# Kernel optimization log

Measured on AMD Instinct MI355X. Metric: run time of the kernel, lower is better.

The kernel has to match this reference:

```python
import jax, jax.numpy as jnp
import numpy as np

EPS = 1e-6

def rmsnorm(x, w):
    # x: (B, N, D), w: (D,)
    var = jnp.mean(jnp.square(x), axis=-1, keepdims=True)
    return x * jax.lax.rsqrt(var + EPS) * w

def head_mixing(x):
    # Parameter-free cross-head mix: split each head's D dims into N chunks
    # and transpose the (head, chunk) axes. x: (B, N, D), D % N == 0.
    B, N, D = x.shape
    c = D // N
    return x.reshape(B, N, N, c).transpose(0, 2, 1, 3).reshape(B, N, D)

def setup_inputs() -> dict:
    key = jax.random.key(0)
    ks = jax.random.split(key, 4)
    B, N, D, H = 8192, 16, 256, 512
    return {
        "x": jax.random.normal(ks[0], (B, N, D), dtype=jnp.float32),
        "norm1_w": jnp.ones((D,), dtype=jnp.float32),
        "norm2_w": jnp.ones((D,), dtype=jnp.float32),
        "w1": jax.random.normal(ks[1], (N, D, H), dtype=jnp.float32) * (1.0 / np.sqrt(D)),
        "w3": jax.random.normal(ks[2], (N, D, H), dtype=jnp.float32) * (1.0 / np.sqrt(D)),
        "w2": jax.random.normal(ks[3], (N, H, D), dtype=jnp.float32) * (1.0 / np.sqrt(H)),
    }

def reference(x, norm1_w, norm2_w, w1, w3, w2):
    # P = HeadMixing(RMSNorm(X)) + X
    p = head_mixing(rmsnorm(x, norm1_w)) + x
    # Q = PerHeadSwiGLUFFN(RMSNorm(P)) + P  (grouped per-head SwiGLU)
    pn = rmsnorm(p, norm2_w)                       # (B, N, D)
    g = jnp.einsum('bnd,ndh->bnh', pn, w1)         # gate proj
    u = jnp.einsum('bnd,ndh->bnh', pn, w3)         # up proj
    h = jax.nn.silu(g) * u                         # (B, N, H)
    q = jnp.einsum('bnh,nhd->bnd', h, w2) + p
    return q
```

## Files before the change

### kernel.cpp

```cpp
#include <hip/hip_runtime.h>
#include <hip/hip_bf16.h>

#define B_ 8192
#define N_ 16
#define D_ 256
#define H_ 512

using bf16x8 = __attribute__((ext_vector_type(8))) short;
using f32x4  = __attribute__((ext_vector_type(4))) float;

__device__ __forceinline__ void gload_lds16(const void* g, void* l) {
    __builtin_amdgcn_global_load_lds(
        (const __attribute__((address_space(1))) void*)g,
        (__attribute__((address_space(3))) void*)l, 16, 0, 0);
}

__device__ __forceinline__ short f2bf(float f) {
    unsigned int u = __float_as_uint(f);
    u += 0x7fffu + ((u >> 16) & 1u);
    return (short)(u >> 16);
}

__global__ __launch_bounds__(256) void k_prep(const float* __restrict__ w1,
                                              const float* __restrict__ w3,
                                              const float* __restrict__ w2,
                                              short* __restrict__ w1t,
                                              short* __restrict__ w3t,
                                              short* __restrict__ w2t) {
    int o = blockIdx.x * 256 + threadIdx.x;
    int n = o >> 17;
    int r = o & 131071;
    int h = r >> 8, d = r & 255;
    w1t[o] = f2bf(w1[(size_t)n * 131072 + (size_t)d * 512 + h]);
    w3t[o] = f2bf(w3[(size_t)n * 131072 + (size_t)d * 512 + h]);
    int d2 = r >> 9, h2 = r & 511;
    w2t[o] = f2bf(w2[(size_t)n * 131072 + (size_t)h2 * 256 + d2]);
}

__global__ __launch_bounds__(256) void k_mix(const float* __restrict__ x,
                                             const float* __restrict__ n1w,
                                             const float* __restrict__ n2w,
                                             float* __restrict__ p_ws,
                                             short* __restrict__ pn_ws) {
    __shared__ float xs[N_ * D_];
    __shared__ float ps[N_ * D_];
    __shared__ float inv1[N_];
    __shared__ float inv2[N_];
    int b = blockIdx.x;
    int t = threadIdx.x;

    const float4* xb4 = (const float4*)(x + (size_t)b * (N_ * D_));
    float4* xs4 = (float4*)xs;
#pragma unroll
    for (int i = 0; i < 4; ++i) xs4[t + i * 256] = xb4[t + i * 256];
    __syncthreads();

    int hh = t >> 4, sub = t & 15;
    float s = 0.f;
#pragma unroll
    for (int j = 0; j < 16; ++j) { float v = xs[hh * 256 + sub * 16 + j]; s += v * v; }
    s += __shfl_xor(s, 1); s += __shfl_xor(s, 2);
    s += __shfl_xor(s, 4); s += __shfl_xor(s, 8);
    if (sub == 0) inv1[hh] = rsqrtf(s * (1.0f / 256.0f) + 1e-6f);
    __syncthreads();

    {
        int n = t >> 4, j = t & 15;
#pragma unroll 1
        for (int m = 0; m < 16; ++m) {
            float v = xs[n * 256 + m * 16 + j] * inv1[n] * n1w[m * 16 + j]
                    + xs[m * 256 + t];
            ps[m * 256 + t] = v;
        }
    }
    __syncthreads();

    float s2 = 0.f;
#pragma unroll
    for (int j = 0; j < 16; ++j) { float v = ps[hh * 256 + sub * 16 + j]; s2 += v * v; }
    s2 += __shfl_xor(s2, 1); s2 += __shfl_xor(s2, 2);
    s2 += __shfl_xor(s2, 4); s2 += __shfl_xor(s2, 8);
    if (sub == 0) inv2[hh] = rsqrtf(s2 * (1.0f / 256.0f) + 1e-6f);
    __syncthreads();

#pragma unroll 1
    for (int m = 0; m < 16; ++m) {
        float v = ps[m * 256 + t];
        size_t off = ((size_t)m * B_ + b) * D_ + t;
        p_ws[off]  = v;
        pn_ws[off] = f2bf(v * inv2[m] * n2w[t]);
    }
}

__global__ __launch_bounds__(256, 2) void k_gateup(const short* __restrict__ pn,
                                                   const short* __restrict__ w1t,
                                                   const short* __restrict__ w3t,
                                                   short* __restrict__ hact) {
    int bid = blockIdx.x;
    int bx = (bid & 7) * 1024 + (bid >> 3);
    int nt = bx & 7;
    int mt = (bx >> 3) & 63;
    int head = bx >> 9;

    __shared__ short As[128 * 32];
    __shared__ short B1s[64 * 32];
    __shared__ short B3s[64 * 32];

    int t = threadIdx.x;
    int wave = t >> 6, lane = t & 63;
    int rowBase = (wave >> 1) * 64;
    int colBase = (wave & 1) * 32;

    f32x4 accG[4][2], accU[4][2];
#pragma unroll
    for (int m = 0; m < 4; ++m)
#pragma unroll
        for (int nn = 0; nn < 2; ++nn) {
            accG[m][nn] = (f32x4){0.f, 0.f, 0.f, 0.f};
            accU[m][nn] = (f32x4){0.f, 0.f, 0.f, 0.f};
        }

    const short* Ab  = pn  + ((size_t)head * B_ + (size_t)mt * 128) * D_;
    const short* B1b = w1t + ((size_t)head * H_ + (size_t)nt * 64) * D_;
    const short* B3b = w3t + ((size_t)head * H_ + (size_t)nt * 64) * D_;

    int lr = t >> 2;
    int lk = (t & 3) * 8;

    for (int k0 = 0; k0 < 256; k0 += 32) {
        gload_lds16(Ab  + (size_t)lr * 256 + k0 + lk,        &As[t * 8]);
        gload_lds16(Ab  + (size_t)(lr + 64) * 256 + k0 + lk, &As[2048 + t * 8]);
        gload_lds16(B1b + (size_t)lr * 256 + k0 + lk,        &B1s[t * 8]);
        gload_lds16(B3b + (size_t)lr * 256 + k0 + lk,        &B3s[t * 8]);
        __syncthreads();

        int kg = (lane >> 4) * 8;
        int l16 = lane & 15;
        bf16x8 aF[4], b1F[2], b3F[2];
#pragma unroll
        for (int m = 0; m < 4; ++m)
            aF[m] = *(const bf16x8*)&As[(rowBase + m * 16 + l16) * 32 + kg];
#pragma unroll
        for (int nn = 0; nn < 2; ++nn) {
            b1F[nn] = *(const bf16x8*)&B1s[(colBase + nn * 16 + l16) * 32 + kg];
            b3F[nn] = *(const bf16x8*)&B3s[(colBase + nn * 16 + l16) * 32 + kg];
        }
#pragma unroll
        for (int m = 0; m < 4; ++m)
#pragma unroll
            for (int nn = 0; nn < 2; ++nn) {
                accG[m][nn] = __builtin_amdgcn_mfma_f32_16x16x32_bf16(
                    aF[m], b1F[nn], accG[m][nn], 0, 0, 0);
                accU[m][nn] = __builtin_amdgcn_mfma_f32_16x16x32_bf16(
                    aF[m], b3F[nn], accU[m][nn], 0, 0, 0);
            }
        __syncthreads();
    }

    int l16 = lane & 15, lrg = (lane >> 4) * 4;
    size_t hbase = (size_t)head * B_ * H_;
#pragma unroll
    for (int m = 0; m < 4; ++m) {
        int row0 = mt * 128 + rowBase + m * 16 + lrg;
#pragma unroll
        for (int nn = 0; nn < 2; ++nn) {
            int col = nt * 64 + colBase + nn * 16 + l16;
#pragma unroll
            for (int r = 0; r < 4; ++r) {
                float g = accG[m][nn][r];
                float u = accU[m][nn][r];
                float hv = g * (1.0f / (1.0f + __expf(-g))) * u;
                hact[hbase + (size_t)(row0 + r) * H_ + col] = f2bf(hv);
            }
        }
    }
}

__global__ __launch_bounds__(256, 2) void k_down(const short* __restrict__ hact,
                                                 const short* __restrict__ w2t,
                                                 const float* __restrict__ p_ws,
                                                 float* __restrict__ out) {
    int bid = blockIdx.x;
    int bx = (bid & 7) * 256 + (bid >> 3);
    int nt = bx & 1;
    int mt = (bx >> 1) & 63;
    int head = bx >> 7;

    __shared__ short As[128 * 32];
    __shared__ short Bs[128 * 32];

    int t = threadIdx.x;
    int wave = t >> 6, lane = t & 63;
    int rowBase = (wave >> 1) * 64;
    int colBase = (wave & 1) * 64;

    f32x4 acc[4][4];
#pragma unroll
    for (int m = 0; m < 4; ++m)
#pragma unroll
        for (int nn = 0; nn < 4; ++nn) acc[m][nn] = (f32x4){0.f, 0.f, 0.f, 0.f};

    const short* Ab = hact + ((size_t)head * B_ + (size_t)mt * 128) * H_;
    const short* Bb = w2t  + ((size_t)head * D_ + (size_t)nt * 128) * H_;

    int lr = t >> 2;
    int lk = (t & 3) * 8;

    for (int k0 = 0; k0 < 512; k0 += 32) {
        gload_lds16(Ab + (size_t)lr * 512 + k0 + lk,        &As[t * 8]);
        gload_lds16(Ab + (size_t)(lr + 64) * 512 + k0 + lk, &As[2048 + t * 8]);
        gload_lds16(Bb + (size_t)lr * 512 + k0 + lk,        &Bs[t * 8]);
        gload_lds16(Bb + (size_t)(lr + 64) * 512 + k0 + lk, &Bs[2048 + t * 8]);
        __syncthreads();

        int kg = (lane >> 4) * 8;
        int l16 = lane & 15;
        bf16x8 aF[4], bF[4];
#pragma unroll
        for (int m = 0; m < 4; ++m)
            aF[m] = *(const bf16x8*)&As[(rowBase + m * 16 + l16) * 32 + kg];
#pragma unroll
        for (int nn = 0; nn < 4; ++nn)
            bF[nn] = *(const bf16x8*)&Bs[(colBase + nn * 16 + l16) * 32 + kg];
#pragma unroll
        for (int m = 0; m < 4; ++m)
#pragma unroll
            for (int nn = 0; nn < 4; ++nn)
                acc[m][nn] = __builtin_amdgcn_mfma_f32_16x16x32_bf16(
                    aF[m], bF[nn], acc[m][nn], 0, 0, 0);
        __syncthreads();
    }

    int l16 = lane & 15, lrg = (lane >> 4) * 4;
#pragma unroll
    for (int m = 0; m < 4; ++m) {
        int row0 = mt * 128 + rowBase + m * 16 + lrg;
#pragma unroll
        for (int nn = 0; nn < 4; ++nn) {
            int col = nt * 128 + colBase + nn * 16 + l16;
#pragma unroll
            for (int r = 0; r < 4; ++r) {
                int row = row0 + r;
                float pv = p_ws[((size_t)head * B_ + row) * D_ + col];
                out[(size_t)row * (N_ * D_) + head * D_ + col] = acc[m][nn][r] + pv;
            }
        }
    }
}

extern "C" void kernel_launch(void* const* d_in, const int* in_sizes, int n_in,
                              void* d_out, int out_size, void* d_ws, size_t ws_size,
                              hipStream_t stream) {
    const float* x   = (const float*)d_in[0];
    const float* n1w = (const float*)d_in[1];
    const float* n2w = (const float*)d_in[2];
    const float* w1  = (const float*)d_in[3];
    const float* w3  = (const float*)d_in[4];
    const float* w2  = (const float*)d_in[5];
    float* out = (float*)d_out;

    char* ws = (char*)d_ws;
    short* w1t  = (short*)(ws);
    short* w3t  = (short*)(ws + (4ull  << 20));
    short* w2t  = (short*)(ws + (8ull  << 20));
    short* pn   = (short*)(ws + (12ull << 20));
    float* p    = (float*)(ws + (76ull << 20));
    short* hact = (short*)(ws + (204ull << 20));

    k_prep<<<(N_ * D_ * H_) / 256, 256, 0, stream>>>(w1, w3, w2, w1t, w3t, w2t);
    k_mix<<<B_, 256, 0, stream>>>(x, n1w, n2w, p, pn);
    k_gateup<<<N_ * (B_ / 128) * (H_ / 64), 256, 0, stream>>>(pn, w1t, w3t, hact);
    k_down<<<N_ * (B_ / 128) * (D_ / 128), 256, 0, stream>>>(hact, w2t, p, out);
}
```

Before: 317.7 us.

## Double-buffer GEMM k-loops with XOR-swizzled LDS and store residual in bf16

Both GEMM kernels now stage 64-wide K tiles into two LDS buffers. The next tile's global-to-LDS loads are issued while MFMAs run on the current one, which halves the barrier count and hides load latency. A XOR swizzle on the 16-byte chunk index is meant to avoid LDS bank conflicts on fragment reads. The residual P is written and read as bf16 instead of fp32 to cut workspace traffic, which adds rounding error to the output residual. The larger LDS footprint (64KB in k_down) may reduce occupancy.

```diff
diff --git a/kernel.cpp b/kernel.cpp
--- a/kernel.cpp
+++ b/kernel.cpp
@@ -19,6 +19,25 @@
     unsigned int u = __float_as_uint(f);
     u += 0x7fffu + ((u >> 16) & 1u);
     return (short)(u >> 16);
+}
+
+__device__ __forceinline__ float bf2f(short s) {
+    return __uint_as_float(((unsigned int)(unsigned short)s) << 16);
+}
+
+template<int ROWS>
+__device__ __forceinline__ void stage_sw(const short* __restrict__ g, int gs,
+                                         short* lds, int t) {
+#pragma unroll
+    for (int rnd = 0; rnd < ROWS / 32; ++rnd) {
+        int dr = rnd * 32 + (t >> 3);
+        int c = (t & 7) ^ (dr & 7);
+        gload_lds16(g + (size_t)dr * gs + c * 8, &lds[rnd * 2048 + t * 8]);
+    }
+}
+
+__device__ __forceinline__ bf16x8 fragsw(const short* buf, int row, int kg) {
+    return *(const bf16x8*)&buf[(row << 6) + (((kg ^ row) & 7) << 3)];
 }
 
 __global__ __launch_bounds__(256) void k_prep(const float* __restrict__ w1,
@@ -40,7 +59,7 @@
 __global__ __launch_bounds__(256) void k_mix(const float* __restrict__ x,
                                              const float* __restrict__ n1w,
                                              const float* __restrict__ n2w,
-                                             float* __restrict__ p_ws,
+                                             short* __restrict__ pb_ws,
                                              short* __restrict__ pn_ws) {
     __shared__ float xs[N_ * D_];
     __shared__ float ps[N_ * D_];
@@ -87,7 +106,7 @@
     for (int m = 0; m < 16; ++m) {
         float v = ps[m * 256 + t];
         size_t off = ((size_t)m * B_ + b) * D_ + t;
-        p_ws[off]  = v;
+        pb_ws[off] = f2bf(v);
         pn_ws[off] = f2bf(v * inv2[m] * n2w[t]);
     }
 }
@@ -102,14 +121,15 @@
     int mt = (bx >> 3) & 63;
     int head = bx >> 9;
 
-    __shared__ short As[128 * 32];
-    __shared__ short B1s[64 * 32];
-    __shared__ short B3s[64 * 32];
+    __shared__ short As[2][128 * 64];
+    __shared__ short B1s[2][64 * 64];
+    __shared__ short B3s[2][64 * 64];
 
     int t = threadIdx.x;
     int wave = t >> 6, lane = t & 63;
     int rowBase = (wave >> 1) * 64;
     int colBase = (wave & 1) * 32;
+    int l16 = lane & 15, kq = lane >> 4;
 
     f32x4 accG[4][2], accU[4][2];
 #pragma unroll
@@ -124,40 +144,50 @@
     const short* B1b = w1t + ((size_t)head * H_ + (size_t)nt * 64) * D_;
     const short* B3b = w3t + ((size_t)head * H_ + (size_t)nt * 64) * D_;
 
-    int lr = t >> 2;
-    int lk = (t & 3) * 8;
-
-    for (int k0 = 0; k0 < 256; k0 += 32) {
-        gload_lds16(Ab  + (size_t)lr * 256 + k0 + lk,        &As[t * 8]);
-        gload_lds16(Ab  + (size_t)(lr + 64) * 256 + k0 + lk, &As[2048 + t * 8]);
-        gload_lds16(B1b + (size_t)lr * 256 + k0 + lk,        &B1s[t * 8]);
-        gload_lds16(B3b + (size_t)lr * 256 + k0 + lk,        &B3s[t * 8]);
-        __syncthreads();
-
-        int kg = (lane >> 4) * 8;
-        int l16 = lane & 15;
-        bf16x8 aF[4], b1F[2], b3F[2];
-#pragma unroll
-        for (int m = 0; m < 4; ++m)
-            aF[m] = *(const bf16x8*)&As[(rowBase + m * 16 + l16) * 32 + kg];
-#pragma unroll
-        for (int nn = 0; nn < 2; ++nn) {
-            b1F[nn] = *(const bf16x8*)&B1s[(colBase + nn * 16 + l16) * 32 + kg];
-            b3F[nn] = *(const bf16x8*)&B3s[(colBase + nn * 16 + l16) * 32 + kg];
-        }
-#pragma unroll
-        for (int m = 0; m < 4; ++m)
+    stage_sw<128>(Ab,  D_, &As[0][0],  t);
+    stage_sw<64> (B1b, D_, &B1s[0][0], t);
+    stage_sw<64> (B3b, D_, &B3s[0][0], t);
+    __syncthreads();
+
+    int cur = 0;
+#pragma unroll
+    for (int kt = 0; kt < 4; ++kt) {
+        if (kt < 3) {
+            int k0 = (kt + 1) * 64;
+            stage_sw<128>(Ab  + k0, D_, &As[cur ^ 1][0],  t);
+            stage_sw<64> (B1b + k0, D_, &B1s[cur ^ 1][0], t);
+            stage_sw<64> (B3b + k0, D_, &B3s[cur ^ 1][0], t);
+        }
+        const short* Ap  = &As[cur][0];
+        const short* B1p = &B1s[cur][0];
+        const short* B3p = &B3s[cur][0];
+#pragma unroll
+        for (int ks = 0; ks < 2; ++ks) {
+            int kg = ks * 4 + kq;
+            bf16x8 aF[4], b1F[2], b3F[2];
+#pragma unroll
+            for (int m = 0; m < 4; ++m)
+                aF[m] = fragsw(Ap, rowBase + m * 16 + l16, kg);
 #pragma unroll
             for (int nn = 0; nn < 2; ++nn) {
-                accG[m][nn] = __builtin_amdgcn_mfma_f32_16x16x32_bf16(
-                    aF[m], b1F[nn], accG[m][nn], 0, 0, 0);
-                accU[m][nn] = __builtin_amdgcn_mfma_f32_16x16x32_bf16(
-                    aF[m], b3F[nn], accU[m][nn], 0, 0, 0);
+                b1F[nn] = fragsw(B1p, colBase + nn * 16 + l16, kg);
+                b3F[nn] = fragsw(B3p, colBase + nn * 16 + l16, kg);
             }
-        __syncthreads();
-    }
-
-    int l16 = lane & 15, lrg = (lane >> 4) * 4;
+#pragma unroll
+            for (int m = 0; m < 4; ++m)
+#pragma unroll
+                for (int nn = 0; nn < 2; ++nn) {
+                    accG[m][nn] = __builtin_amdgcn_mfma_f32_16x16x32_bf16(
+                        aF[m], b1F[nn], accG[m][nn], 0, 0, 0);
+                    accU[m][nn] = __builtin_amdgcn_mfma_f32_16x16x32_bf16(
+                        aF[m], b3F[nn], accU[m][nn], 0, 0, 0);
+                }
+        }
+        if (kt < 3) __syncthreads();
+        cur ^= 1;
+    }
+
+    int lrg = (lane >> 4) * 4;
     size_t hbase = (size_t)head * B_ * H_;
 #pragma unroll
     for (int m = 0; m < 4; ++m) {
@@ -178,7 +208,7 @@
 
 __global__ __launch_bounds__(256, 2) void k_down(const short* __restrict__ hact,
                                                  const short* __restrict__ w2t,
-                                                 const float* __restrict__ p_ws,
+                                                 const short* __restrict__ pb,
                                                  float* __restrict__ out) {
     int bid = blockIdx.x;
     int bx = (bid & 7) * 256 + (bid >> 3);
@@ -186,13 +216,14 @@
     int mt = (bx >> 1) & 63;
     int head = bx >> 7;
 
-    __shared__ short As[128 * 32];
-    __shared__ short Bs[128 * 32];
+    __shared__ short As[2][128 * 64];
+    __shared__ short Bs[2][128 * 64];
 
     int t = threadIdx.x;
     int wave = t >> 6, lane = t & 63;
     int rowBase = (wave >> 1) * 64;
     int colBase = (wave & 1) * 64;
+    int l16 = lane & 15, kq = lane >> 4;
 
     f32x4 acc[4][4];
 #pragma unroll
@@ -203,35 +234,42 @@
     const short* Ab = hact + ((size_t)head * B_ + (size_t)mt * 128) * H_;
     const short* Bb = w2t  + ((size_t)head * D_ + (size_t)nt * 128) * H_;
 
-    int lr = t >> 2;
-    int lk = (t & 3) * 8;
-
-    for (int k0 = 0; k0 < 512; k0 += 32) {
-        gload_lds16(Ab + (size_t)lr * 512 + k0 + lk,        &As[t * 8]);
-        gload_lds16(Ab + (size_t)(lr + 64) * 512 + k0 + lk, &As[2048 + t * 8]);
-        gload_lds16(Bb + (size_t)lr * 512 + k0 + lk,        &Bs[t * 8]);
-        gload_lds16(Bb + (size_t)(lr + 64) * 512 + k0 + lk, &Bs[2048 + t * 8]);
-        __syncthreads();
-
-        int kg = (lane >> 4) * 8;
-        int l16 = lane & 15;
-        bf16x8 aF[4], bF[4];
-#pragma unroll
-        for (int m = 0; m < 4; ++m)
-            aF[m] = *(const bf16x8*)&As[(rowBase + m * 16 + l16) * 32 + kg];
-#pragma unroll
-        for (int nn = 0; nn < 4; ++nn)
-            bF[nn] = *(const bf16x8*)&Bs[(colBase + nn * 16 + l16) * 32 + kg];
-#pragma unroll
-        for (int m = 0; m < 4; ++m)
+    stage_sw<128>(Ab, H_, &As[0][0], t);
+    stage_sw<128>(Bb, H_, &Bs[0][0], t);
+    __syncthreads();
+
+    int cur = 0;
+#pragma unroll
+    for (int kt = 0; kt < 8; ++kt) {
+        if (kt < 7) {
+            int k0 = (kt + 1) * 64;
+            stage_sw<128>(Ab + k0, H_, &As[cur ^ 1][0], t);
+            stage_sw<128>(Bb + k0, H_, &Bs[cur ^ 1][0], t);
+        }
+        const short* Ap = &As[cur][0];
+        const short* Bp = &Bs[cur][0];
+#pragma unroll
+        for (int ks = 0; ks < 2; ++ks) {
+            int kg = ks * 4 + kq;
+            bf16x8 aF[4], bF[4];
+#pragma unroll
+            for (int m = 0; m < 4; ++m)
+                aF[m] = fragsw(Ap, rowBase + m * 16 + l16, kg);
 #pragma unroll
             for (int nn = 0; nn < 4; ++nn)
-                acc[m][nn] = __builtin_amdgcn_mfma_f32_16x16x32_bf16(
-                    aF[m], bF[nn], acc[m][nn], 0, 0, 0);
-        __syncthreads();
-    }
-
-    int l16 = lane & 15, lrg = (lane >> 4) * 4;
+                bF[nn] = fragsw(Bp, colBase + nn * 16 + l16, kg);
+#pragma unroll
+            for (int m = 0; m < 4; ++m)
+#pragma unroll
+                for (int nn = 0; nn < 4; ++nn)
+                    acc[m][nn] = __builtin_amdgcn_mfma_f32_16x16x32_bf16(
+                        aF[m], bF[nn], acc[m][nn], 0, 0, 0);
+        }
+        if (kt < 7) __syncthreads();
+        cur ^= 1;
+    }
+
+    int lrg = (lane >> 4) * 4;
 #pragma unroll
     for (int m = 0; m < 4; ++m) {
         int row0 = mt * 128 + rowBase + m * 16 + lrg;
@@ -241,7 +279,7 @@
 #pragma unroll
             for (int r = 0; r < 4; ++r) {
                 int row = row0 + r;
-                float pv = p_ws[((size_t)head * B_ + row) * D_ + col];
+                float pv = bf2f(pb[((size_t)head * B_ + row) * D_ + col]);
                 out[(size_t)row * (N_ * D_) + head * D_ + col] = acc[m][nn][r] + pv;
             }
         }
@@ -264,11 +302,11 @@
     short* w3t  = (short*)(ws + (4ull  << 20));
     short* w2t  = (short*)(ws + (8ull  << 20));
     short* pn   = (short*)(ws + (12ull << 20));
-    float* p    = (float*)(ws + (76ull << 20));
-    short* hact = (short*)(ws + (204ull << 20));
+    short* pb   = (short*)(ws + (76ull << 20));
+    short* hact = (short*)(ws + (140ull << 20));
 
     k_prep<<<(N_ * D_ * H_) / 256, 256, 0, stream>>>(w1, w3, w2, w1t, w3t, w2t);
-    k_mix<<<B_, 256, 0, stream>>>(x, n1w, n2w, p, pn);
+    k_mix<<<B_, 256, 0, stream>>>(x, n1w, n2w, pb, pn);
     k_gateup<<<N_ * (B_ / 128) * (H_ / 64), 256, 0, stream>>>(pn, w1t, w3t, hact);
-    k_down<<<N_ * (B_ / 128) * (D_ / 128), 256, 0, stream>>>(hact, w2t, p, out);
-}
+    k_down<<<N_ * (B_ / 128) * (D_ / 128), 256, 0, stream>>>(hact, w2t, pb, out);
+}
```

New measurement: 312.9 us. No clear change (-1.5%).

## Fuse gate/up and down projections into one kernel with hidden activations in LDS

Applied to the files above, without the earlier changes.

Merges the gate/up GEMM and the down GEMM into a single per-head kernel. Each block handles 64 rows, keeps the SiLU-gated hidden activations in shared memory, and never writes them to global memory. Weights are repacked so gate and up tiles for each 64-column chunk sit next to each other. Tiles are staged into XOR-swizzled, double-buffered LDS, and the down projection's two K-halves are combined with an LDS reduction. The residual P is now stored as bf16 instead of fp32 to cut traffic. In exchange, the kernel uses 128 KB of dynamic LDS, which limits occupancy, and the residual loses precision.

```diff
diff --git a/kernel.cpp b/kernel.cpp
--- a/kernel.cpp
+++ b/kernel.cpp
@@ -21,18 +21,41 @@
     return (short)(u >> 16);
 }
 
+__device__ __forceinline__ float bf2f(short s) {
+    return __uint_as_float(((unsigned int)(unsigned short)s) << 16);
+}
+
+__device__ __forceinline__ unsigned int pack2(float lo, float hi) {
+    return (unsigned int)(unsigned short)f2bf(lo)
+         | ((unsigned int)(unsigned short)f2bf(hi) << 16);
+}
+
+template<int ROWS, int GRANS>
+__device__ __forceinline__ void stage_g(const short* __restrict__ g, int gstride,
+                                        int colBase, short* lds, int t) {
+#pragma unroll
+    for (int rnd = 0; rnd < (ROWS * GRANS) / 512; ++rnd) {
+        int flat = rnd * 512 + t;
+        int dr = flat / GRANS;
+        int gd = flat % GRANS;
+        int sg = (gd & ~7) | ((gd ^ dr) & 7);
+        gload_lds16(g + (size_t)dr * gstride + colBase + sg * 8, &lds[flat * 8]);
+    }
+}
+
 __global__ __launch_bounds__(256) void k_prep(const float* __restrict__ w1,
                                               const float* __restrict__ w3,
                                               const float* __restrict__ w2,
-                                              short* __restrict__ w1t,
-                                              short* __restrict__ w3t,
+                                              short* __restrict__ wgu,
                                               short* __restrict__ w2t) {
     int o = blockIdx.x * 256 + threadIdx.x;
     int n = o >> 17;
     int r = o & 131071;
     int h = r >> 8, d = r & 255;
-    w1t[o] = f2bf(w1[(size_t)n * 131072 + (size_t)d * 512 + h]);
-    w3t[o] = f2bf(w3[(size_t)n * 131072 + (size_t)d * 512 + h]);
+    size_t g1 = ((size_t)(n * 8 + (h >> 6)) * 128
+                 + ((h >> 4) & 3) * 32 + (h & 15)) * 256 + d;
+    wgu[g1]        = f2bf(w1[(size_t)n * 131072 + (size_t)d * 512 + h]);
+    wgu[g1 + 4096] = f2bf(w3[(size_t)n * 131072 + (size_t)d * 512 + h]);
     int d2 = r >> 9, h2 = r & 511;
     w2t[o] = f2bf(w2[(size_t)n * 131072 + (size_t)h2 * 256 + d2]);
 }
@@ -40,7 +63,7 @@
 __global__ __launch_bounds__(256) void k_mix(const float* __restrict__ x,
                                              const float* __restrict__ n1w,
                                              const float* __restrict__ n2w,
-                                             float* __restrict__ p_ws,
+                                             short* __restrict__ pb_ws,
                                              short* __restrict__ pn_ws) {
     __shared__ float xs[N_ * D_];
     __shared__ float ps[N_ * D_];
@@ -87,164 +110,179 @@
     for (int m = 0; m < 16; ++m) {
         float v = ps[m * 256 + t];
         size_t off = ((size_t)m * B_ + b) * D_ + t;
-        p_ws[off]  = v;
+        pb_ws[off] = f2bf(v);
         pn_ws[off] = f2bf(v * inv2[m] * n2w[t]);
     }
 }
 
-__global__ __launch_bounds__(256, 2) void k_gateup(const short* __restrict__ pn,
-                                                   const short* __restrict__ w1t,
-                                                   const short* __restrict__ w3t,
-                                                   short* __restrict__ hact) {
-    int bid = blockIdx.x;
-    int bx = (bid & 7) * 1024 + (bid >> 3);
-    int nt = bx & 7;
-    int mt = (bx >> 3) & 63;
-    int head = bx >> 9;
-
-    __shared__ short As[128 * 32];
-    __shared__ short B1s[64 * 32];
-    __shared__ short B3s[64 * 32];
-
-    int t = threadIdx.x;
-    int wave = t >> 6, lane = t & 63;
-    int rowBase = (wave >> 1) * 64;
-    int colBase = (wave & 1) * 32;
-
-    f32x4 accG[4][2], accU[4][2];
-#pragma unroll
-    for (int m = 0; m < 4; ++m)
-#pragma unroll
-        for (int nn = 0; nn < 2; ++nn) {
-            accG[m][nn] = (f32x4){0.f, 0.f, 0.f, 0.f};
-            accU[m][nn] = (f32x4){0.f, 0.f, 0.f, 0.f};
-        }
-
-    const short* Ab  = pn  + ((size_t)head * B_ + (size_t)mt * 128) * D_;
-    const short* B1b = w1t + ((size_t)head * H_ + (size_t)nt * 64) * D_;
-    const short* B3b = w3t + ((size_t)head * H_ + (size_t)nt * 64) * D_;
-
-    int lr = t >> 2;
-    int lk = (t & 3) * 8;
-
-    for (int k0 = 0; k0 < 256; k0 += 32) {
-        gload_lds16(Ab  + (size_t)lr * 256 + k0 + lk,        &As[t * 8]);
-        gload_lds16(Ab  + (size_t)(lr + 64) * 256 + k0 + lk, &As[2048 + t * 8]);
-        gload_lds16(B1b + (size_t)lr * 256 + k0 + lk,        &B1s[t * 8]);
-        gload_lds16(B3b + (size_t)lr * 256 + k0 + lk,        &B3s[t * 8]);
-        __syncthreads();
-
-        int kg = (lane >> 4) * 8;
-        int l16 = lane & 15;
-        bf16x8 aF[4], b1F[2], b3F[2];
-#pragma unroll
-        for (int m = 0; m < 4; ++m)
-            aF[m] = *(const bf16x8*)&As[(rowBase + m * 16 + l16) * 32 + kg];
-#pragma unroll
-        for (int nn = 0; nn < 2; ++nn) {
-            b1F[nn] = *(const bf16x8*)&B1s[(colBase + nn * 16 + l16) * 32 + kg];
-            b3F[nn] = *(const bf16x8*)&B3s[(colBase + nn * 16 + l16) * 32 + kg];
-        }
-#pragma unroll
-        for (int m = 0; m < 4; ++m)
-#pragma unroll
-            for (int nn = 0; nn < 2; ++nn) {
-                accG[m][nn] = __builtin_amdgcn_mfma_f32_16x16x32_bf16(
-                    aF[m], b1F[nn], accG[m][nn], 0, 0, 0);
-                accU[m][nn] = __builtin_amdgcn_mfma_f32_16x16x32_bf16(
-                    aF[m], b3F[nn], accU[m][nn], 0, 0, 0);
-            }
-        __syncthreads();
-    }
-
-    int l16 = lane & 15, lrg = (lane >> 4) * 4;
-    size_t hbase = (size_t)head * B_ * H_;
-#pragma unroll
-    for (int m = 0; m < 4; ++m) {
-        int row0 = mt * 128 + rowBase + m * 16 + lrg;
-#pragma unroll
-        for (int nn = 0; nn < 2; ++nn) {
-            int col = nt * 64 + colBase + nn * 16 + l16;
-#pragma unroll
-            for (int r = 0; r < 4; ++r) {
-                float g = accG[m][nn][r];
-                float u = accU[m][nn][r];
-                float hv = g * (1.0f / (1.0f + __expf(-g))) * u;
-                hact[hbase + (size_t)(row0 + r) * H_ + col] = f2bf(hv);
-            }
-        }
-    }
-}
-
-__global__ __launch_bounds__(256, 2) void k_down(const short* __restrict__ hact,
-                                                 const short* __restrict__ w2t,
-                                                 const float* __restrict__ p_ws,
-                                                 float* __restrict__ out) {
+__global__ __launch_bounds__(512, 2) void k_ffn(const short* __restrict__ pn,
+                                                const short* __restrict__ wgu,
+                                                const short* __restrict__ w2t,
+                                                const short* __restrict__ pb,
+                                                float* __restrict__ out) {
+    extern __shared__ char smem[];
+    short* sbuf0 = (short*)smem;
+    short* sbuf1 = (short*)(smem + 32768);
+    short* hact  = (short*)(smem + 65536);
+    float* red   = (float*)smem;
+
     int bid = blockIdx.x;
     int bx = (bid & 7) * 256 + (bid >> 3);
-    int nt = bx & 1;
-    int mt = (bx >> 1) & 63;
     int head = bx >> 7;
-
-    __shared__ short As[128 * 32];
-    __shared__ short Bs[128 * 32];
+    int mtB = (bx & 127) * 64;
 
     int t = threadIdx.x;
-    int wave = t >> 6, lane = t & 63;
-    int rowBase = (wave >> 1) * 64;
-    int colBase = (wave & 1) * 64;
-
-    f32x4 acc[4][4];
-#pragma unroll
-    for (int m = 0; m < 4; ++m)
-#pragma unroll
-        for (int nn = 0; nn < 4; ++nn) acc[m][nn] = (f32x4){0.f, 0.f, 0.f, 0.f};
-
-    const short* Ab = hact + ((size_t)head * B_ + (size_t)mt * 128) * H_;
-    const short* Bb = w2t  + ((size_t)head * D_ + (size_t)nt * 128) * H_;
-
-    int lr = t >> 2;
-    int lk = (t & 3) * 8;
-
-    for (int k0 = 0; k0 < 512; k0 += 32) {
-        gload_lds16(Ab + (size_t)lr * 512 + k0 + lk,        &As[t * 8]);
-        gload_lds16(Ab + (size_t)(lr + 64) * 512 + k0 + lk, &As[2048 + t * 8]);
-        gload_lds16(Bb + (size_t)lr * 512 + k0 + lk,        &Bs[t * 8]);
-        gload_lds16(Bb + (size_t)(lr + 64) * 512 + k0 + lk, &Bs[2048 + t * 8]);
+    int w = t >> 6, lane = t & 63;
+    int l16 = lane & 15, kq = lane >> 4;
+
+    const short* wguH = wgu + (size_t)head * (8 * 128 * 256);
+    const short* w2H  = w2t + (size_t)head * (D_ * H_);
+
+    int mg = w >> 2;
+    int hg = w & 3;
+
+    bf16x8 P[2][8];
+#pragma unroll
+    for (int mf = 0; mf < 2; ++mf) {
+        const short* prow = pn + ((size_t)head * B_ + mtB + mg * 32 + mf * 16 + l16) * D_;
+#pragma unroll
+        for (int kt = 0; kt < 8; ++kt)
+            P[mf][kt] = *(const bf16x8*)(prow + kt * 32 + kq * 8);
+    }
+
+    stage_g<128, 16>(wguH, 256, 0, sbuf0, t);
+    __syncthreads();
+
+    int rowG = hg * 32 + l16;
+    int rowU = rowG + 16;
+
+#pragma unroll 1
+    for (int c = 0; c < 8; ++c) {
+        const short* cbase = wguH + (size_t)c * (128 * 256);
+        f32x4 aG[2], aU[2];
+#pragma unroll
+        for (int mf = 0; mf < 2; ++mf) {
+            aG[mf] = (f32x4){0.f, 0.f, 0.f, 0.f};
+            aU[mf] = (f32x4){0.f, 0.f, 0.f, 0.f};
+        }
+        stage_g<128, 16>(cbase, 256, 128, sbuf1, t);
+#pragma unroll
+        for (int kt = 0; kt < 4; ++kt) {
+            int g = kt * 4 + kq;
+            int gpg = (g & 8) | ((g ^ rowG) & 7);
+            int gpu = (g & 8) | ((g ^ rowU) & 7);
+            bf16x8 fG = *(const bf16x8*)&sbuf0[rowG * 128 + gpg * 8];
+            bf16x8 fU = *(const bf16x8*)&sbuf0[rowU * 128 + gpu * 8];
+#pragma unroll
+            for (int mf = 0; mf < 2; ++mf) {
+                aG[mf] = __builtin_amdgcn_mfma_f32_16x16x32_bf16(fG, P[mf][kt], aG[mf], 0, 0, 0);
+                aU[mf] = __builtin_amdgcn_mfma_f32_16x16x32_bf16(fU, P[mf][kt], aU[mf], 0, 0, 0);
+            }
+        }
         __syncthreads();
-
-        int kg = (lane >> 4) * 8;
-        int l16 = lane & 15;
-        bf16x8 aF[4], bF[4];
-#pragma unroll
-        for (int m = 0; m < 4; ++m)
-            aF[m] = *(const bf16x8*)&As[(rowBase + m * 16 + l16) * 32 + kg];
-#pragma unroll
-        for (int nn = 0; nn < 4; ++nn)
-            bF[nn] = *(const bf16x8*)&Bs[(colBase + nn * 16 + l16) * 32 + kg];
-#pragma unroll
-        for (int m = 0; m < 4; ++m)
-#pragma unroll
-            for (int nn = 0; nn < 4; ++nn)
-                acc[m][nn] = __builtin_amdgcn_mfma_f32_16x16x32_bf16(
-                    aF[m], bF[nn], acc[m][nn], 0, 0, 0);
+        if (c < 7)
+            stage_g<128, 16>(cbase + 128 * 256, 256, 0, sbuf0, t);
+#pragma unroll
+        for (int kt = 0; kt < 4; ++kt) {
+            int g = kt * 4 + kq;
+            int gpg = (g & 8) | ((g ^ rowG) & 7);
+            int gpu = (g & 8) | ((g ^ rowU) & 7);
+            bf16x8 fG = *(const bf16x8*)&sbuf1[rowG * 128 + gpg * 8];
+            bf16x8 fU = *(const bf16x8*)&sbuf1[rowU * 128 + gpu * 8];
+#pragma unroll
+            for (int mf = 0; mf < 2; ++mf) {
+                aG[mf] = __builtin_amdgcn_mfma_f32_16x16x32_bf16(fG, P[mf][4 + kt], aG[mf], 0, 0, 0);
+                aU[mf] = __builtin_amdgcn_mfma_f32_16x16x32_bf16(fU, P[mf][4 + kt], aU[mf], 0, 0, 0);
+            }
+        }
+#pragma unroll
+        for (int mf = 0; mf < 2; ++mf) {
+            float hv[4];
+#pragma unroll
+            for (int r = 0; r < 4; ++r) {
+                float g = aG[mf][r];
+                float u = aU[mf][r];
+                hv[r] = g * (1.0f / (1.0f + __expf(-g))) * u;
+            }
+            int m = mg * 32 + mf * 16 + l16;
+            int gr = c * 8 + hg * 2 + (kq >> 1);
+            int gp = (gr & ~7) | ((gr ^ m) & 7);
+            int sidx = m * 512 + gp * 8 + (kq & 1) * 4;
+            *(unsigned int*)&hact[sidx]     = pack2(hv[0], hv[1]);
+            *(unsigned int*)&hact[sidx + 2] = pack2(hv[2], hv[3]);
+        }
         __syncthreads();
     }
 
-    int l16 = lane & 15, lrg = (lane >> 4) * 4;
-#pragma unroll
-    for (int m = 0; m < 4; ++m) {
-        int row0 = mt * 128 + rowBase + m * 16 + lrg;
-#pragma unroll
-        for (int nn = 0; nn < 4; ++nn) {
-            int col = nt * 128 + colBase + nn * 16 + l16;
-#pragma unroll
-            for (int r = 0; r < 4; ++r) {
-                int row = row0 + r;
-                float pv = p_ws[((size_t)head * B_ + row) * D_ + col];
-                out[(size_t)row * (N_ * D_) + head * D_ + col] = acc[m][nn][r] + pv;
-            }
-        }
+    int dg = w >> 1;
+    int ks = w & 1;
+
+    f32x4 accB[4][4];
+#pragma unroll
+    for (int mf = 0; mf < 4; ++mf)
+#pragma unroll
+        for (int df = 0; df < 4; ++df) accB[mf][df] = (f32x4){0.f, 0.f, 0.f, 0.f};
+
+    stage_g<256, 8>(w2H, 512, 0, sbuf0, t);
+    __syncthreads();
+
+#pragma unroll 1
+    for (int c = 0; c < 8; ++c) {
+        short* cur = (c & 1) ? sbuf1 : sbuf0;
+        short* nxt = (c & 1) ? sbuf0 : sbuf1;
+        if (c < 7) stage_g<256, 8>(w2H, 512, (c + 1) * 64, nxt, t);
+
+        bf16x8 aH[4], bW[4];
+#pragma unroll
+        for (int mf = 0; mf < 4; ++mf) {
+            int m = mf * 16 + l16;
+            int gr = c * 8 + ks * 4 + kq;
+            int gp = (gr & ~7) | ((gr ^ m) & 7);
+            aH[mf] = *(const bf16x8*)&hact[m * 512 + gp * 8];
+        }
+#pragma unroll
+        for (int df = 0; df < 4; ++df) {
+            int d = dg * 64 + df * 16 + l16;
+            int gp = ((ks * 4 + kq) ^ d) & 7;
+            bW[df] = *(const bf16x8*)&cur[d * 64 + gp * 8];
+        }
+#pragma unroll
+        for (int mf = 0; mf < 4; ++mf)
+#pragma unroll
+            for (int df = 0; df < 4; ++df)
+                accB[mf][df] = __builtin_amdgcn_mfma_f32_16x16x32_bf16(
+                    aH[mf], bW[df], accB[mf][df], 0, 0, 0);
+        __syncthreads();
+    }
+
+    if (ks == 1) {
+#pragma unroll
+        for (int mf = 0; mf < 4; ++mf)
+#pragma unroll
+            for (int df = 0; df < 4; ++df)
+#pragma unroll
+                for (int r = 0; r < 4; ++r) {
+                    int m = mf * 16 + kq * 4 + r;
+                    int dl = df * 16 + l16;
+                    red[dg * 4096 + m * 64 + dl] = accB[mf][df][r];
+                }
+    }
+    __syncthreads();
+    if (ks == 0) {
+#pragma unroll
+        for (int mf = 0; mf < 4; ++mf)
+#pragma unroll
+            for (int df = 0; df < 4; ++df)
+#pragma unroll
+                for (int r = 0; r < 4; ++r) {
+                    int m = mf * 16 + kq * 4 + r;
+                    int dl = df * 16 + l16;
+                    int d = dg * 64 + dl;
+                    int row = mtB + m;
+                    float v = accB[mf][df][r] + red[dg * 4096 + m * 64 + dl];
+                    v += bf2f(pb[((size_t)head * B_ + row) * D_ + d]);
+                    out[(size_t)row * (N_ * D_) + head * D_ + d] = v;
+                }
     }
 }
 
@@ -260,15 +298,15 @@
     float* out = (float*)d_out;
 
     char* ws = (char*)d_ws;
-    short* w1t  = (short*)(ws);
-    short* w3t  = (short*)(ws + (4ull  << 20));
-    short* w2t  = (short*)(ws + (8ull  << 20));
-    short* pn   = (short*)(ws + (12ull << 20));
-    float* p    = (float*)(ws + (76ull << 20));
-    short* hact = (short*)(ws + (204ull << 20));
-
-    k_prep<<<(N_ * D_ * H_) / 256, 256, 0, stream>>>(w1, w3, w2, w1t, w3t, w2t);
-    k_mix<<<B_, 256, 0, stream>>>(x, n1w, n2w, p, pn);
-    k_gateup<<<N_ * (B_ / 128) * (H_ / 64), 256, 0, stream>>>(pn, w1t, w3t, hact);
-    k_down<<<N_ * (B_ / 128) * (D_ / 128), 256, 0, stream>>>(hact, w2t, p, out);
-}
+    short* wgu = (short*)(ws);
+    short* w2t = (short*)(ws + (8ull  << 20));
+    short* pn  = (short*)(ws + (12ull << 20));
+    short* pb  = (short*)(ws + (76ull << 20));
+
+    (void)hipFuncSetAttribute((const void*)k_ffn,
+                              hipFuncAttributeMaxDynamicSharedMemorySize, 131072);
+
+    k_prep<<<(N_ * D_ * H_) / 256, 256, 0, stream>>>(w1, w3, w2, wgu, w2t);
+    k_mix<<<B_, 256, 0, stream>>>(x, n1w, n2w, pb, pn);
+    k_ffn<<<N_ * (B_ / 64), 512, 131072, stream>>>(pn, wgu, w2t, pb, out);
+}
```

After: 317.7 us. Within noise of the previous version (+0.0%).

## Rewrite GEMMs with 256x256 tiles, double-buffered swizzled LDS, interleaved gate/up weights

Applied to the files above, without the earlier changes.

Both GEMM kernels move to a shared core with 512 threads, 256x256 output tiles, K-step 64, double-buffered LDS staging (128KB dynamic) and an XOR swizzle to avoid bank conflicts. Gate and up weights are interleaved in 16-row groups so a single B tile feeds both projections. The residual P is now stored as bf16 instead of fp32, which halves that workspace traffic but loses precision in the residual add. The larger tiles cut global reloads of the operands but leave fewer blocks per GPU and put more pressure on registers.

```diff
diff --git a/kernel.cpp b/kernel.cpp
--- a/kernel.cpp
+++ b/kernel.cpp
@@ -21,18 +21,114 @@
     return (short)(u >> 16);
 }
 
+__device__ __forceinline__ float bf2f(short s) {
+    return __uint_as_float(((unsigned int)(unsigned short)s) << 16);
+}
+
+__device__ __forceinline__ f32x4 mfma(bf16x8 a, bf16x8 b, f32x4 c) {
+    return __builtin_amdgcn_mfma_f32_16x16x32_bf16(a, b, c, 0, 0, 0);
+}
+
+__device__ __forceinline__ void stage_ab(const short* __restrict__ Ag, int sA,
+                                         const short* __restrict__ Bg, int sB,
+                                         int k0, short* Al, short* Bl, int t) {
+#pragma unroll
+    for (int rnd = 0; rnd < 4; ++rnd) {
+        int flat = rnd * 512 + t;
+        int row = flat >> 3, g = flat & 7;
+        int sg = (g ^ row) & 7;
+        gload_lds16(Ag + (size_t)row * sA + k0 + sg * 8, Al + flat * 8);
+    }
+#pragma unroll
+    for (int rnd = 0; rnd < 4; ++rnd) {
+        int flat = rnd * 512 + t;
+        int row = flat >> 3, g = flat & 7;
+        int sg = (g ^ row) & 7;
+        gload_lds16(Bg + (size_t)row * sB + k0 + sg * 8, Bl + flat * 8);
+    }
+}
+
+__device__ __forceinline__ bf16x8 rdfrag(const short* base, int row, int g) {
+    int gp = (g ^ row) & 7;
+    return *(const bf16x8*)&base[(row << 6) + (gp << 3)];
+}
+
+template<int NT>
+__device__ __forceinline__ void gemm_core(const short* __restrict__ Ag, int sA,
+                                          const short* __restrict__ Bg, int sB,
+                                          short* lds, f32x4 (&acc)[8][4],
+                                          int t, int rowA0, int rowB0) {
+    int lane = t & 63;
+    int l16 = lane & 15, kq = lane >> 4;
+
+    stage_ab(Ag, sA, Bg, sB, 0, lds, lds + 32768, t);
+    __syncthreads();
+
+#pragma unroll 1
+    for (int kt = 0; kt < NT; ++kt) {
+        short* Asl = lds + (kt & 1) * 16384;
+        short* Bsl = lds + 32768 + (kt & 1) * 16384;
+        if (kt + 1 < NT)
+            stage_ab(Ag, sA, Bg, sB, (kt + 1) * 64,
+                     lds + ((kt + 1) & 1) * 16384,
+                     lds + 32768 + ((kt + 1) & 1) * 16384, t);
+
+        bf16x8 aF[4], bF[4];
+#pragma unroll
+        for (int j = 0; j < 4; ++j)
+            bF[j] = rdfrag(Bsl, rowB0 + j * 16 + l16, kq);
+#pragma unroll
+        for (int i = 0; i < 4; ++i)
+            aF[i] = rdfrag(Asl, rowA0 + i * 16 + l16, kq);
+#pragma unroll
+        for (int i = 0; i < 4; ++i)
+#pragma unroll
+            for (int j = 0; j < 4; ++j)
+                acc[i][j] = mfma(aF[i], bF[j], acc[i][j]);
+#pragma unroll
+        for (int i = 0; i < 4; ++i)
+            aF[i] = rdfrag(Asl, rowA0 + 64 + i * 16 + l16, kq);
+#pragma unroll
+        for (int i = 0; i < 4; ++i)
+#pragma unroll
+            for (int j = 0; j < 4; ++j)
+                acc[4 + i][j] = mfma(aF[i], bF[j], acc[4 + i][j]);
+#pragma unroll
+        for (int j = 0; j < 4; ++j)
+            bF[j] = rdfrag(Bsl, rowB0 + j * 16 + l16, 4 + kq);
+#pragma unroll
+        for (int i = 0; i < 4; ++i)
+            aF[i] = rdfrag(Asl, rowA0 + i * 16 + l16, 4 + kq);
+#pragma unroll
+        for (int i = 0; i < 4; ++i)
+#pragma unroll
+            for (int j = 0; j < 4; ++j)
+                acc[i][j] = mfma(aF[i], bF[j], acc[i][j]);
+#pragma unroll
+        for (int i = 0; i < 4; ++i)
+            aF[i] = rdfrag(Asl, rowA0 + 64 + i * 16 + l16, 4 + kq);
+#pragma unroll
+        for (int i = 0; i < 4; ++i)
+#pragma unroll
+            for (int j = 0; j < 4; ++j)
+                acc[4 + i][j] = mfma(aF[i], bF[j], acc[4 + i][j]);
+
+        __syncthreads();
+    }
+}
+
 __global__ __launch_bounds__(256) void k_prep(const float* __restrict__ w1,
                                               const float* __restrict__ w3,
                                               const float* __restrict__ w2,
-                                              short* __restrict__ w1t,
-                                              short* __restrict__ w3t,
+                                              short* __restrict__ wgu,
                                               short* __restrict__ w2t) {
     int o = blockIdx.x * 256 + threadIdx.x;
     int n = o >> 17;
     int r = o & 131071;
     int h = r >> 8, d = r & 255;
-    w1t[o] = f2bf(w1[(size_t)n * 131072 + (size_t)d * 512 + h]);
-    w3t[o] = f2bf(w3[(size_t)n * 131072 + (size_t)d * 512 + h]);
+    size_t base = ((size_t)n * 1024 + (h >> 4) * 32 + (h & 15)) * 256 + d;
+    wgu[base]            = f2bf(w1[(size_t)n * 131072 + (size_t)d * 512 + h]);
+    wgu[base + 16 * 256] = f2bf(w3[(size_t)n * 131072 + (size_t)d * 512 + h]);
     int d2 = r >> 9, h2 = r & 511;
     w2t[o] = f2bf(w2[(size_t)n * 131072 + (size_t)h2 * 256 + d2]);
 }
@@ -40,7 +136,7 @@
 __global__ __launch_bounds__(256) void k_mix(const float* __restrict__ x,
                                              const float* __restrict__ n1w,
                                              const float* __restrict__ n2w,
-                                             float* __restrict__ p_ws,
+                                             short* __restrict__ pb_ws,
                                              short* __restrict__ pn_ws) {
     __shared__ float xs[N_ * D_];
     __shared__ float ps[N_ * D_];
@@ -87,162 +183,96 @@
     for (int m = 0; m < 16; ++m) {
         float v = ps[m * 256 + t];
         size_t off = ((size_t)m * B_ + b) * D_ + t;
-        p_ws[off]  = v;
+        pb_ws[off] = f2bf(v);
         pn_ws[off] = f2bf(v * inv2[m] * n2w[t]);
     }
 }
 
-__global__ __launch_bounds__(256, 2) void k_gateup(const short* __restrict__ pn,
-                                                   const short* __restrict__ w1t,
-                                                   const short* __restrict__ w3t,
-                                                   short* __restrict__ hact) {
+__global__ __launch_bounds__(512, 2) void k_gu(const short* __restrict__ pn,
+                                               const short* __restrict__ wgu,
+                                               short* __restrict__ hact) {
+    extern __shared__ char smem[];
+    short* lds = (short*)smem;
+
     int bid = blockIdx.x;
-    int bx = (bid & 7) * 1024 + (bid >> 3);
-    int nt = bx & 7;
-    int mt = (bx >> 3) & 63;
-    int head = bx >> 9;
-
-    __shared__ short As[128 * 32];
-    __shared__ short B1s[64 * 32];
-    __shared__ short B3s[64 * 32];
+    int bx = (bid & 7) * 256 + (bid >> 3);
+    int head = bx >> 7;
+    int mt = (bx >> 2) & 31;
+    int nt = bx & 3;
 
     int t = threadIdx.x;
-    int wave = t >> 6, lane = t & 63;
-    int rowBase = (wave >> 1) * 64;
-    int colBase = (wave & 1) * 32;
-
-    f32x4 accG[4][2], accU[4][2];
-#pragma unroll
-    for (int m = 0; m < 4; ++m)
-#pragma unroll
-        for (int nn = 0; nn < 2; ++nn) {
-            accG[m][nn] = (f32x4){0.f, 0.f, 0.f, 0.f};
-            accU[m][nn] = (f32x4){0.f, 0.f, 0.f, 0.f};
-        }
-
-    const short* Ab  = pn  + ((size_t)head * B_ + (size_t)mt * 128) * D_;
-    const short* B1b = w1t + ((size_t)head * H_ + (size_t)nt * 64) * D_;
-    const short* B3b = w3t + ((size_t)head * H_ + (size_t)nt * 64) * D_;
-
-    int lr = t >> 2;
-    int lk = (t & 3) * 8;
-
-    for (int k0 = 0; k0 < 256; k0 += 32) {
-        gload_lds16(Ab  + (size_t)lr * 256 + k0 + lk,        &As[t * 8]);
-        gload_lds16(Ab  + (size_t)(lr + 64) * 256 + k0 + lk, &As[2048 + t * 8]);
-        gload_lds16(B1b + (size_t)lr * 256 + k0 + lk,        &B1s[t * 8]);
-        gload_lds16(B3b + (size_t)lr * 256 + k0 + lk,        &B3s[t * 8]);
-        __syncthreads();
-
-        int kg = (lane >> 4) * 8;
-        int l16 = lane & 15;
-        bf16x8 aF[4], b1F[2], b3F[2];
-#pragma unroll
-        for (int m = 0; m < 4; ++m)
-            aF[m] = *(const bf16x8*)&As[(rowBase + m * 16 + l16) * 32 + kg];
-#pragma unroll
-        for (int nn = 0; nn < 2; ++nn) {
-            b1F[nn] = *(const bf16x8*)&B1s[(colBase + nn * 16 + l16) * 32 + kg];
-            b3F[nn] = *(const bf16x8*)&B3s[(colBase + nn * 16 + l16) * 32 + kg];
-        }
-#pragma unroll
-        for (int m = 0; m < 4; ++m)
-#pragma unroll
-            for (int nn = 0; nn < 2; ++nn) {
-                accG[m][nn] = __builtin_amdgcn_mfma_f32_16x16x32_bf16(
-                    aF[m], b1F[nn], accG[m][nn], 0, 0, 0);
-                accU[m][nn] = __builtin_amdgcn_mfma_f32_16x16x32_bf16(
-                    aF[m], b3F[nn], accU[m][nn], 0, 0, 0);
-            }
-        __syncthreads();
-    }
-
-    int l16 = lane & 15, lrg = (lane >> 4) * 4;
-    size_t hbase = (size_t)head * B_ * H_;
-#pragma unroll
-    for (int m = 0; m < 4; ++m) {
-        int row0 = mt * 128 + rowBase + m * 16 + lrg;
-#pragma unroll
-        for (int nn = 0; nn < 2; ++nn) {
-            int col = nt * 64 + colBase + nn * 16 + l16;
+    int w = t >> 6, lane = t & 63;
+    int l16 = lane & 15, kq = lane >> 4;
+    int wm = w >> 2, wn = w & 3;
+
+    f32x4 acc[8][4];
+#pragma unroll
+    for (int i = 0; i < 8; ++i)
+#pragma unroll
+        for (int j = 0; j < 4; ++j) acc[i][j] = (f32x4){0.f, 0.f, 0.f, 0.f};
+
+    const short* Ag = pn  + ((size_t)head * B_ + (size_t)mt * 256) * D_;
+    const short* Bg = wgu + ((size_t)head * 1024 + (size_t)nt * 256) * D_;
+
+    gemm_core<4>(Ag, D_, Bg, D_, lds, acc, t, wm * 128, wn * 64);
+
+    size_t hb = (size_t)head * B_ * H_;
+#pragma unroll
+    for (int mf = 0; mf < 8; ++mf) {
+        int m = mt * 256 + wm * 128 + mf * 16 + kq * 4;
+#pragma unroll
+        for (int p = 0; p < 2; ++p) {
+            int h = (nt * 8 + wn * 2 + p) * 16 + l16;
 #pragma unroll
             for (int r = 0; r < 4; ++r) {
-                float g = accG[m][nn][r];
-                float u = accU[m][nn][r];
+                float g = acc[mf][2 * p][r];
+                float u = acc[mf][2 * p + 1][r];
                 float hv = g * (1.0f / (1.0f + __expf(-g))) * u;
-                hact[hbase + (size_t)(row0 + r) * H_ + col] = f2bf(hv);
+                hact[hb + (size_t)(m + r) * H_ + h] = f2bf(hv);
             }
         }
     }
 }
 
-__global__ __launch_bounds__(256, 2) void k_down(const short* __restrict__ hact,
-                                                 const short* __restrict__ w2t,
-                                                 const float* __restrict__ p_ws,
-                                                 float* __restrict__ out) {
+__global__ __launch_bounds__(512, 2) void k_dn(const short* __restrict__ hact,
+                                               const short* __restrict__ w2t,
+                                               const short* __restrict__ pb,
+                                               float* __restrict__ out) {
+    extern __shared__ char smem[];
+    short* lds = (short*)smem;
+
     int bid = blockIdx.x;
-    int bx = (bid & 7) * 256 + (bid >> 3);
-    int nt = bx & 1;
-    int mt = (bx >> 1) & 63;
-    int head = bx >> 7;
-
-    __shared__ short As[128 * 32];
-    __shared__ short Bs[128 * 32];
+    int bx = (bid & 7) * 64 + (bid >> 3);
+    int head = bx >> 5;
+    int mt = bx & 31;
 
     int t = threadIdx.x;
-    int wave = t >> 6, lane = t & 63;
-    int rowBase = (wave >> 1) * 64;
-    int colBase = (wave & 1) * 64;
-
-    f32x4 acc[4][4];
-#pragma unroll
-    for (int m = 0; m < 4; ++m)
-#pragma unroll
-        for (int nn = 0; nn < 4; ++nn) acc[m][nn] = (f32x4){0.f, 0.f, 0.f, 0.f};
-
-    const short* Ab = hact + ((size_t)head * B_ + (size_t)mt * 128) * H_;
-    const short* Bb = w2t  + ((size_t)head * D_ + (size_t)nt * 128) * H_;
-
-    int lr = t >> 2;
-    int lk = (t & 3) * 8;
-
-    for (int k0 = 0; k0 < 512; k0 += 32) {
-        gload_lds16(Ab + (size_t)lr * 512 + k0 + lk,        &As[t * 8]);
-        gload_lds16(Ab + (size_t)(lr + 64) * 512 + k0 + lk, &As[2048 + t * 8]);
-        gload_lds16(Bb + (size_t)lr * 512 + k0 + lk,        &Bs[t * 8]);
-        gload_lds16(Bb + (size_t)(lr + 64) * 512 + k0 + lk, &Bs[2048 + t * 8]);
-        __syncthreads();
-
-        int kg = (lane >> 4) * 8;
-        int l16 = lane & 15;
-        bf16x8 aF[4], bF[4];
-#pragma unroll
-        for (int m = 0; m < 4; ++m)
-            aF[m] = *(const bf16x8*)&As[(rowBase + m * 16 + l16) * 32 + kg];
-#pragma unroll
-        for (int nn = 0; nn < 4; ++nn)
-            bF[nn] = *(const bf16x8*)&Bs[(colBase + nn * 16 + l16) * 32 + kg];
-#pragma unroll
-        for (int m = 0; m < 4; ++m)
-#pragma unroll
-            for (int nn = 0; nn < 4; ++nn)
-                acc[m][nn] = __builtin_amdgcn_mfma_f32_16x16x32_bf16(
-                    aF[m], bF[nn], acc[m][nn], 0, 0, 0);
-        __syncthreads();
-    }
-
-    int l16 = lane & 15, lrg = (lane >> 4) * 4;
-#pragma unroll
-    for (int m = 0; m < 4; ++m) {
-        int row0 = mt * 128 + rowBase + m * 16 + lrg;
-#pragma unroll
-        for (int nn = 0; nn < 4; ++nn) {
-            int col = nt * 128 + colBase + nn * 16 + l16;
+    int w = t >> 6, lane = t & 63;
+    int l16 = lane & 15, kq = lane >> 4;
+    int wm = w >> 2, wn = w & 3;
+
+    f32x4 acc[8][4];
+#pragma unroll
+    for (int i = 0; i < 8; ++i)
+#pragma unroll
+        for (int j = 0; j < 4; ++j) acc[i][j] = (f32x4){0.f, 0.f, 0.f, 0.f};
+
+    const short* Ag = hact + ((size_t)head * B_ + (size_t)mt * 256) * H_;
+    const short* Bg = w2t  + (size_t)head * D_ * H_;
+
+    gemm_core<8>(Ag, H_, Bg, H_, lds, acc, t, wm * 128, wn * 64);
+
+#pragma unroll
+    for (int mf = 0; mf < 8; ++mf) {
+        int m = mt * 256 + wm * 128 + mf * 16 + kq * 4;
+#pragma unroll
+        for (int nf = 0; nf < 4; ++nf) {
+            int d = wn * 64 + nf * 16 + l16;
 #pragma unroll
             for (int r = 0; r < 4; ++r) {
-                int row = row0 + r;
-                float pv = p_ws[((size_t)head * B_ + row) * D_ + col];
-                out[(size_t)row * (N_ * D_) + head * D_ + col] = acc[m][nn][r] + pv;
+                float v = acc[mf][nf][r]
+                        + bf2f(pb[((size_t)head * B_ + m + r) * D_ + d]);
+                out[(size_t)(m + r) * (N_ * D_) + head * D_ + d] = v;
             }
         }
     }
@@ -260,15 +290,19 @@
     float* out = (float*)d_out;
 
     char* ws = (char*)d_ws;
-    short* w1t  = (short*)(ws);
-    short* w3t  = (short*)(ws + (4ull  << 20));
-    short* w2t  = (short*)(ws + (8ull  << 20));
-    short* pn   = (short*)(ws + (12ull << 20));
-    float* p    = (float*)(ws + (76ull << 20));
-    short* hact = (short*)(ws + (204ull << 20));
-
-    k_prep<<<(N_ * D_ * H_) / 256, 256, 0, stream>>>(w1, w3, w2, w1t, w3t, w2t);
-    k_mix<<<B_, 256, 0, stream>>>(x, n1w, n2w, p, pn);
-    k_gateup<<<N_ * (B_ / 128) * (H_ / 64), 256, 0, stream>>>(pn, w1t, w3t, hact);
-    k_down<<<N_ * (B_ / 128) * (D_ / 128), 256, 0, stream>>>(hact, w2t, p, out);
-}
+    short* wgu  = (short*)(ws);
+    short* w2t  = (short*)(ws + (8ull   << 20));
+    short* pn   = (short*)(ws + (12ull  << 20));
+    short* pb   = (short*)(ws + (76ull  << 20));
+    short* hact = (short*)(ws + (140ull << 20));
+
+    (void)hipFuncSetAttribute((const void*)k_gu,
+                              hipFuncAttributeMaxDynamicSharedMemorySize, 131072);
+    (void)hipFuncSetAttribute((const void*)k_dn,
+                              hipFuncAttributeMaxDynamicSharedMemorySize, 131072);
+
+    k_prep<<<(N_ * D_ * H_) / 256, 256, 0, stream>>>(w1, w3, w2, wgu, w2t);
+    k_mix<<<B_, 256, 0, stream>>>(x, n1w, n2w, pb, pn);
+    k_gu<<<N_ * (B_ / 256) * 4, 512, 131072, stream>>>(pn, wgu, hact);
+    k_dn<<<N_ * (B_ / 256), 512, 131072, stream>>>(hact, w2t, pb, out);
+}
```

New measurement: 296.7 us. 1.07x faster.
